# Optimization experiments

Measured on AMD Instinct MI355X. Metric: run time of the kernel, lower is better.

The kernel has to match this reference:

```python
import jax, jax.numpy as jnp
import numpy as np

D_MODEL = 1024
NUM_HEADS = 16
D_K = D_MODEL // NUM_HEADS  # 64
MAX_SEQ_LEN = 2048
THETA = 10000.0
BATCH = 2
SEQ = 2048


def _rope_tables():
    # freqs: [d_k/2], positions: [max_seq_len] -> angles [max_seq_len, d_k/2]
    freqs = THETA ** (-jnp.arange(0, D_K, 2, dtype=jnp.float32) / D_K)
    positions = jnp.arange(MAX_SEQ_LEN, dtype=jnp.float32)[:, None]
    angles = positions * freqs[None, :]
    return jnp.cos(angles), jnp.sin(angles)


def _apply_rope(x, token_positions, cos_cached, sin_cached):
    # x: [..., seq, d_k]; token_positions: [seq]
    cos = cos_cached[token_positions]  # [seq, d_k/2]
    sin = sin_cached[token_positions]
    x_even = x[..., ::2]
    x_odd = x[..., 1::2]
    r_even = x_even * cos - x_odd * sin
    r_odd = x_even * sin + x_odd * cos
    # interleave even/odd back into last dim
    out = jnp.stack([r_even, r_odd], axis=-1)
    return out.reshape(x.shape)


def setup_inputs() -> dict:
    key = jax.random.key(0)
    ks = jax.random.split(key, 5)
    scale = 1.0 / np.sqrt(D_MODEL)
    in_features = jax.random.normal(ks[0], (BATCH, SEQ, D_MODEL), dtype=jnp.float32)
    q_proj = jax.random.normal(ks[1], (D_MODEL, D_MODEL), dtype=jnp.float32) * scale
    k_proj = jax.random.normal(ks[2], (D_MODEL, D_MODEL), dtype=jnp.float32) * scale
    v_proj = jax.random.normal(ks[3], (D_MODEL, D_MODEL), dtype=jnp.float32) * scale
    o_proj = jax.random.normal(ks[4], (D_MODEL, D_MODEL), dtype=jnp.float32) * scale
    mask = jnp.tril(jnp.ones((SEQ, SEQ), dtype=bool))  # causal
    token_positions = jnp.arange(SEQ, dtype=jnp.int32)
    return {
        "in_features": in_features,
        "q_proj": q_proj,
        "k_proj": k_proj,
        "v_proj": v_proj,
        "o_proj": o_proj,
        "mask": mask,
        "token_positions": token_positions,
    }


def reference(in_features, q_proj, k_proj, v_proj, o_proj, mask, token_positions):
    B, S, _ = in_features.shape
    cos_cached, sin_cached = _rope_tables()
    # fused QKV projection (same math as x @ cat(Wq,Wk,Wv).T then chunk)
    q = jnp.einsum("bsd,ed->bse", in_features, q_proj)
    k = jnp.einsum("bsd,ed->bse", in_features, k_proj)
    v = jnp.einsum("bsd,ed->bse", in_features, v_proj)
    # ... seq (h d) -> ... h seq d
    q = q.reshape(B, S, NUM_HEADS, D_K).transpose(0, 2, 1, 3)
    k = k.reshape(B, S, NUM_HEADS, D_K).transpose(0, 2, 1, 3)
    v = v.reshape(B, S, NUM_HEADS, D_K).transpose(0, 2, 1, 3)
    q = _apply_rope(q, token_positions, cos_cached, sin_cached)
    k = _apply_rope(k, token_positions, cos_cached, sin_cached)
    scores = jnp.einsum("bhqd,bhkd->bhqk", q, k) / np.sqrt(D_K)
    scores = jnp.where(mask, scores, -jnp.inf)
    attn = jax.nn.softmax(scores, axis=-1)
    out = jnp.einsum("bhqk,bhkd->bhqd", attn, v)
    # ... h seq d -> ... seq (h d)
    concat = out.transpose(0, 2, 1, 3).reshape(B, S, D_MODEL)
    return jnp.einsum("bsd,ed->bse", concat, o_proj)
```

## Files before the change

### kernel.cpp

```cpp
#include <hip/hip_runtime.h>
#include <cstdint>

#define D_MODEL 1024
#define NHEADS 16
#define DKH 64
#define SEQL 2048
#define NBATCH 2
#define NROWS (NBATCH * SEQL)

typedef __bf16 bf16;
typedef __bf16 bf16x2 __attribute__((ext_vector_type(2)));
typedef __bf16 bf16x4 __attribute__((ext_vector_type(4)));
typedef __bf16 bf16x8 __attribute__((ext_vector_type(8)));
typedef float f32x4 __attribute__((ext_vector_type(4)));
typedef float f32x16 __attribute__((ext_vector_type(16)));
typedef unsigned u32x4 __attribute__((ext_vector_type(4)));

static __device__ __forceinline__ f32x4 mfma16(bf16x8 a, bf16x8 b, f32x4 c) {
  return __builtin_amdgcn_mfma_f32_16x16x32_bf16(a, b, c, 0, 0, 0);
}

static __device__ __forceinline__ f32x16 mfma32(bf16x8 a, bf16x8 b, f32x16 c) {
  return __builtin_amdgcn_mfma_f32_32x32x16_bf16(a, b, c, 0, 0, 0);
}

static __device__ __forceinline__ void gload_lds16(const bf16* g, bf16* l) {
  __builtin_amdgcn_global_load_lds(
      (const __attribute__((address_space(1))) void*)g,
      (__attribute__((address_space(3))) void*)l, 16, 0, 0);
}

static __device__ __forceinline__ float fexp2(float x) {
  return __builtin_amdgcn_exp2f(x);
}

static __device__ __forceinline__ unsigned cvt_pk(float a, float b) {
  unsigned r;
  asm("v_cvt_pk_bf16_f32 %0, %1, %2" : "=v"(r) : "v"(a), "v"(b));
  return r;
}

static __device__ __forceinline__ void plswap(unsigned& a, unsigned& b) {
  asm("v_permlane32_swap_b32 %0, %1" : "+v"(a), "+v"(b));
}

__global__ __launch_bounds__(256) void convert_kernel(
    const float* __restrict__ x, const float* __restrict__ wq,
    const float* __restrict__ wk, const float* __restrict__ wv,
    const float* __restrict__ wo, bf16* __restrict__ xb,
    bf16* __restrict__ wqb, bf16* __restrict__ wkb, bf16* __restrict__ wvb,
    bf16* __restrict__ wob) {
  int i4 = blockIdx.x * 256 + threadIdx.x;
  const float* src;
  bf16* dst;
  int off;
  if (i4 < (NROWS * D_MODEL / 4)) {
    src = x; dst = xb; off = i4;
  } else {
    int j = i4 - NROWS * D_MODEL / 4;
    int sel = j >> 18;
    off = j & ((1 << 18) - 1);
    src = sel == 0 ? wq : sel == 1 ? wk : sel == 2 ? wv : wo;
    dst = sel == 0 ? wqb : sel == 1 ? wkb : sel == 2 ? wvb : wob;
  }
  float4 v = ((const float4*)src)[off];
  bf16x4 o;
  o[0] = (bf16)v.x; o[1] = (bf16)v.y; o[2] = (bf16)v.z; o[3] = (bf16)v.w;
  ((bf16x4*)dst)[off] = o;
}

__global__ __launch_bounds__(256, 3) void qkv_gemm(
    const bf16* __restrict__ A, const bf16* __restrict__ Bq,
    const bf16* __restrict__ Bk, const bf16* __restrict__ Bv,
    const int* __restrict__ tpos, bf16* __restrict__ Qb,
    bf16* __restrict__ Kb, bf16* __restrict__ Vt) {
  __shared__ bf16 As[128 * 64];
  __shared__ bf16 Bs[3][64 * 64];
  const int t = threadIdx.x, wave = t >> 6, lane = t & 63;
  const int quad = lane >> 4, l16 = lane & 15;
  const int bm = blockIdx.x * 128, bn = blockIdx.y * 64;

  f32x4 acc[3][2][4];
  for (int o = 0; o < 3; o++)
    for (int mt = 0; mt < 2; mt++)
      for (int nt = 0; nt < 4; nt++)
        for (int r = 0; r < 4; r++) acc[o][mt][nt][r] = 0.0f;

  for (int k0 = 0; k0 < D_MODEL; k0 += 64) {
    for (int j = 0; j < 4; j++) {
      int s = (wave * 4 + j) * 64 + lane;
      int srow = s >> 3, scol = (s & 7) ^ (srow & 7);
      gload_lds16(&A[(size_t)(bm + srow) * D_MODEL + k0 + scol * 8],
                  &As[(wave * 4 + j) * 512]);
    }
    for (int j = 0; j < 2; j++) {
      int s = (wave * 2 + j) * 64 + lane;
      int srow = s >> 3, scol = (s & 7) ^ (srow & 7);
      size_t goff = (size_t)(bn + srow) * D_MODEL + k0 + scol * 8;
      gload_lds16(&Bq[goff], &Bs[0][(wave * 2 + j) * 512]);
      gload_lds16(&Bk[goff], &Bs[1][(wave * 2 + j) * 512]);
      gload_lds16(&Bv[goff], &Bs[2][(wave * 2 + j) * 512]);
    }
    __syncthreads();
    for (int kh = 0; kh < 2; kh++) {
      const int kc = kh * 4 + quad;
      bf16x8 af[2];
      for (int mt = 0; mt < 2; mt++) {
        int row = wave * 32 + mt * 16 + l16;
        af[mt] = *(bf16x8*)&As[row * 64 + (kc ^ (row & 7)) * 8];
      }
      for (int nt = 0; nt < 4; nt++) {
        int row = nt * 16 + l16;
        int off = row * 64 + (kc ^ (row & 7)) * 8;
        bf16x8 bq = *(bf16x8*)&Bs[0][off];
        bf16x8 bk = *(bf16x8*)&Bs[1][off];
        bf16x8 bv = *(bf16x8*)&Bs[2][off];
        for (int mt = 0; mt < 2; mt++) {
          acc[0][mt][nt] = mfma16(af[mt], bq, acc[0][mt][nt]);
          acc[1][mt][nt] = mfma16(af[mt], bk, acc[1][mt][nt]);
          acc[2][mt][nt] = mfma16(af[mt], bv, acc[2][mt][nt]);
        }
      }
    }
    __syncthreads();
  }

  const float qsc = 0.125f * 1.44269504f;
  float freqv[4], sgn[4];
  for (int nt = 0; nt < 4; nt++) {
    int cp = (bn + nt * 16 + l16) & 63;
    freqv[nt] = fexp2((float)(cp >> 1) * -0.41524101f);
    sgn[nt] = (cp & 1) ? 1.0f : -1.0f;
  }
  for (int mt = 0; mt < 2; mt++) {
    int row0 = bm + wave * 32 + mt * 16 + quad * 4;
    for (int r = 0; r < 4; r++) {
      int row = row0 + r;
      float pos = (float)tpos[row & (SEQL - 1)];
      for (int nt = 0; nt < 4; nt++) {
        int col = bn + nt * 16 + l16;
        float sn, cs;
        __sincosf(pos * freqv[nt], &sn, &cs);
        float vq = acc[0][mt][nt][r];
        float vk = acc[1][mt][nt][r];
        float pq = __shfl_xor(vq, 1);
        float pk = __shfl_xor(vk, 1);
        float rq = vq * cs + sgn[nt] * pq * sn;
        float rk = vk * cs + sgn[nt] * pk * sn;
        Qb[(size_t)row * D_MODEL + col] = (bf16)(rq * qsc);
        Kb[(size_t)row * D_MODEL + col] = (bf16)rk;
      }
    }
    for (int nt = 0; nt < 4; nt++) {
      int col = bn + nt * 16 + l16;
      bf16x4 pv;
      for (int r = 0; r < 4; r++) pv[r] = (bf16)acc[2][mt][nt][r];
      *(bf16x4*)&Vt[(size_t)col * NROWS + row0] = pv;
    }
  }
}

template <int BM, int BN, typename OutT>
__device__ __forceinline__ void gemm_body64(const bf16* __restrict__ A,
                                            const bf16* __restrict__ Bm,
                                            OutT* __restrict__ C, int bm,
                                            int bn, int N, int K) {
  constexpr int MT = BM / 32, NT = BN / 32;
  constexpr int CA = BM / 32, CB = BN / 32;
  __shared__ bf16 As[BM * 64];
  __shared__ bf16 Bs[BN * 64];
  const int t = threadIdx.x;
  const int wave = t >> 6, lane = t & 63;
  const int quad = lane >> 4, l16 = lane & 15;
  const int wm = (wave >> 1) * (MT * 16), wn = (wave & 1) * (NT * 16);

  f32x4 acc[MT][NT];
  for (int i = 0; i < MT; i++)
    for (int j = 0; j < NT; j++)
      for (int r = 0; r < 4; r++) acc[i][j][r] = 0.0f;

  for (int k0 = 0; k0 < K; k0 += 64) {
    for (int j = 0; j < CA; j++) {
      int s = (wave * CA + j) * 64 + lane;
      int srow = s >> 3, scol = (s & 7) ^ (srow & 7);
      gload_lds16(&A[(size_t)(bm + srow) * K + k0 + scol * 8],
                  &As[(wave * CA + j) * 512]);
    }
    for (int j = 0; j < CB; j++) {
      int s = (wave * CB + j) * 64 + lane;
      int srow = s >> 3, scol = (s & 7) ^ (srow & 7);
      gload_lds16(&Bm[(size_t)(bn + srow) * K + k0 + scol * 8],
                  &Bs[(wave * CB + j) * 512]);
    }
    __syncthreads();
    for (int kh = 0; kh < 2; kh++) {
      const int kc = kh * 4 + quad;
      bf16x8 af[MT], bfr[NT];
      for (int mt = 0; mt < MT; mt++) {
        int row = wm + mt * 16 + l16;
        af[mt] = *(bf16x8*)&As[row * 64 + (kc ^ (row & 7)) * 8];
      }
      for (int nt = 0; nt < NT; nt++) {
        int row = wn + nt * 16 + l16;
        bfr[nt] = *(bf16x8*)&Bs[row * 64 + (kc ^ (row & 7)) * 8];
      }
      for (int mt = 0; mt < MT; mt++)
        for (int nt = 0; nt < NT; nt++)
          acc[mt][nt] = mfma16(af[mt], bfr[nt], acc[mt][nt]);
    }
    __syncthreads();
  }
  for (int mt = 0; mt < MT; mt++)
    for (int nt = 0; nt < NT; nt++)
      for (int r = 0; r < 4; r++) {
        int row = bm + wm + mt * 16 + quad * 4 + r;
        int col = bn + wn + nt * 16 + l16;
        C[(size_t)row * N + col] = (OutT)acc[mt][nt][r];
      }
}

__global__ __launch_bounds__(256, 3) void o_gemm(const bf16* __restrict__ A,
                                                 const bf16* __restrict__ Bm,
                                                 float* __restrict__ C) {
  gemm_body64<64, 128, float>(A, Bm, C, blockIdx.x * 64, blockIdx.y * 128,
                              D_MODEL, D_MODEL);
}

__global__ __launch_bounds__(256) void attn_kernel(
    const bf16* __restrict__ Q, const bf16* __restrict__ K,
    const bf16* __restrict__ Vt_g, float* __restrict__ O0,
    float* __restrict__ O1, float* __restrict__ O2, float* __restrict__ O3,
    float* __restrict__ L0, float* __restrict__ L1, float* __restrict__ L2,
    float* __restrict__ L3) {
  const int t = threadIdx.x;
  const int wave = t >> 6, lane = t & 63;
  const int l32 = lane & 31, hi = lane >> 5;

  const int id = blockIdx.x;
  const int bh = id & 31;
  const int c = 39 - (id >> 5);
  int qt, piece, np;
  if (c < 4)       { qt = c;                 piece = 0;            np = 1; }
  else if (c < 12) { int e = c - 4;  qt = 4 + (e >> 1); piece = e & 1; np = 2; }
  else if (c < 24) { int e = c - 12; qt = 8 + e / 3;    piece = e % 3; np = 3; }
  else             { int e = c - 24; qt = 12 + (e >> 2); piece = e & 3; np = 4; }
  const int total = qt + 1, bas = total / np, rem = total % np;
  const int len = bas + (piece < rem ? 1 : 0);
  const int k0 = piece * bas + (piece < rem ? piece : rem);
  const int k1 = k0 + len - 1;

  const int b = bh >> 4, h = bh & 15;
  const int q_base = qt * 128;
  const size_t base = (size_t)b * SEQL * D_MODEL + h * DKH;

  __shared__ bf16 Ks[128 * 64];
  __shared__ bf16 Vts[64 * 128];

  const int r8 = lane >> 3, c8 = lane & 7;
  const int r16 = lane >> 4, c16 = lane & 15;

  for (int i = 0; i < 4; i++) {
    int row = wave * 32 + i * 8 + r8;
    int sc = c8 ^ (row & 7);
    gload_lds16(&Q[base + (size_t)(q_base + row) * D_MODEL + sc * 8],
                &Ks[(wave * 32 + i * 8) * 64]);
  }
  __syncthreads();
  bf16x8 qb[4];
  {
    int row = wave * 32 + l32;
#pragma unroll
    for (int ks = 0; ks < 4; ks++) {
      int ch = (ks * 2 + hi) ^ (row & 7);
      qb[ks] = *(bf16x8*)&Ks[row * 64 + ch * 8];
    }
  }
  __syncthreads();

  f32x16 oaccT[2];
  float lsum = 0.0f;
#pragma unroll
  for (int dt = 0; dt < 2; dt++)
#pragma unroll
    for (int r = 0; r < 16; r++) oaccT[dt][r] = 0.0f;

  const bf16* Vrow0 = &Vt_g[(size_t)(h * 64) * NROWS + b * SEQL];

  for (int kv = k0; kv <= k1; kv++) {
    const int kv_base = kv * 128;
    for (int i = 0; i < 4; i++) {
      int row = wave * 32 + i * 8 + r8;
      int sc = c8 ^ (row & 7);
      gload_lds16(&K[base + (size_t)(kv_base + row) * D_MODEL + sc * 8],
                  &Ks[(wave * 32 + i * 8) * 64]);
    }
    for (int i = 0; i < 4; i++) {
      int d = wave * 16 + i * 4 + r16;
      int sc = c16 ^ (d & 7);
      gload_lds16(&Vrow0[(size_t)d * NROWS + kv_base + sc * 8],
                  &Vts[(wave * 16 + i * 4) * 128]);
    }
    __syncthreads();

    const bool diag = (kv == qt);
#pragma unroll
    for (int cc = 0; cc < 4; cc++) {
      f32x16 sT;
#pragma unroll
      for (int r = 0; r < 16; r++) sT[r] = 0.0f;
      {
        int krow = cc * 32 + l32;
#pragma unroll
        for (int ks = 0; ks < 4; ks++) {
          int ch = (ks * 2 + hi) ^ (krow & 7);
          bf16x8 kf = *(bf16x8*)&Ks[krow * 64 + ch * 8];
          sT = mfma32(kf, qb[ks], sT);
        }
      }
      if (diag) {
        int q_loc = wave * 32 + l32;
#pragma unroll
        for (int r = 0; r < 16; r++) {
          int key = cc * 32 + (r & 3) + 8 * (r >> 2) + 4 * hi;
          if (key > q_loc) sT[r] = -1e30f;
        }
      }
      float p[16];
#pragma unroll
      for (int r = 0; r < 16; r++) p[r] = fexp2(sT[r]);
      lsum += (((p[0] + p[1]) + (p[2] + p[3])) +
               ((p[4] + p[5]) + (p[6] + p[7]))) +
              (((p[8] + p[9]) + (p[10] + p[11])) +
               ((p[12] + p[13]) + (p[14] + p[15])));
      unsigned a0 = cvt_pk(p[0], p[1]),  a1 = cvt_pk(p[2], p[3]);
      unsigned b0 = cvt_pk(p[4], p[5]),  b1 = cvt_pk(p[6], p[7]);
      unsigned c0 = cvt_pk(p[8], p[9]),  c1 = cvt_pk(p[10], p[11]);
      unsigned d0 = cvt_pk(p[12], p[13]), d1 = cvt_pk(p[14], p[15]);
      plswap(a0, b0); plswap(a1, b1); plswap(c0, d0); plswap(c1, d1);
      bf16x8 pf[2];
      {
        u32x4 u = {a0, a1, b0, b1};
        pf[0] = __builtin_bit_cast(bf16x8, u);
      }
      {
        u32x4 u = {c0, c1, d0, d1};
        pf[1] = __builtin_bit_cast(bf16x8, u);
      }
#pragma unroll
      for (int dt = 0; dt < 2; dt++) {
        int d = dt * 32 + l32;
#pragma unroll
        for (int ks = 0; ks < 2; ks++) {
          int ch = (cc * 4 + ks * 2 + hi) ^ (d & 7);
          bf16x8 vf = *(bf16x8*)&Vts[d * 128 + ch * 8];
          oaccT[dt] = mfma32(vf, pf[ks], oaccT[dt]);
        }
      }
    }
    __syncthreads();
  }

  lsum += __shfl_xor(lsum, 32);
  float* Ob;
  float* Lb;
  int rbase, roff;
  if (piece == 0)      { Ob = O0; Lb = L0; rbase = SEQL;        roff = 0; }
  else if (piece == 1) { Ob = O1; Lb = L1; rbase = SEQL - 512;  roff = 512; }
  else if (piece == 2) { Ob = O2; Lb = L2; rbase = SEQL - 1024; roff = 1024; }
  else                 { Ob = O3; Lb = L3; rbase = SEQL - 1536; roff = 1536; }
  {
    int qrow = q_base + wave * 32 + l32;
    size_t orow = (size_t)b * rbase + (qrow - roff);
    if (hi == 0) Lb[orow * NHEADS + h] = lsum;
#pragma unroll
    for (int dt = 0; dt < 2; dt++)
#pragma unroll
      for (int rq = 0; rq < 4; rq++) {
        f32x4 vv = {oaccT[dt][rq * 4 + 0], oaccT[dt][rq * 4 + 1],
                    oaccT[dt][rq * 4 + 2], oaccT[dt][rq * 4 + 3]};
        *(f32x4*)&Ob[orow * D_MODEL + h * DKH + dt * 32 + rq * 8 + hi * 4] =
            vv;
      }
  }
}

__global__ __launch_bounds__(256) void normalize_kernel(
    const float* __restrict__ O0, const float* __restrict__ O1,
    const float* __restrict__ O2, const float* __restrict__ O3,
    const float* __restrict__ L0, const float* __restrict__ L1,
    const float* __restrict__ L2, const float* __restrict__ L3,
    bf16* __restrict__ Cc) {
  int i4 = blockIdx.x * 256 + threadIdx.x;
  int row = i4 >> 8;
  int c0 = (i4 & 255) * 4;
  int s = row & (SEQL - 1);
  int b = row >> 11;
  int h = c0 >> 6;
  float l = L0[(size_t)row * NHEADS + h];
  f32x4 v = *(const f32x4*)&O0[(size_t)row * D_MODEL + c0];
  if (s >= 512) {
    size_t r1 = (size_t)b * (SEQL - 512) + (s - 512);
    l += L1[r1 * NHEADS + h];
    f32x4 u = *(const f32x4*)&O1[r1 * D_MODEL + c0];
    for (int r = 0; r < 4; r++) v[r] += u[r];
  }
  if (s >= 1024) {
    size_t r2 = (size_t)b * (SEQL - 1024) + (s - 1024);
    l += L2[r2 * NHEADS + h];
    f32x4 u = *(const f32x4*)&O2[r2 * D_MODEL + c0];
    for (int r = 0; r < 4; r++) v[r] += u[r];
  }
  if (s >= 1536) {
    size_t r3 = (size_t)b * (SEQL - 1536) + (s - 1536);
    l += L3[r3 * NHEADS + h];
    f32x4 u = *(const f32x4*)&O3[r3 * D_MODEL + c0];
    for (int r = 0; r < 4; r++) v[r] += u[r];
  }
  float inv = 1.0f / l;
  bf16x4 o;
  o[0] = (bf16)(v[0] * inv);
  o[1] = (bf16)(v[1] * inv);
  o[2] = (bf16)(v[2] * inv);
  o[3] = (bf16)(v[3] * inv);
  *(bf16x4*)&Cc[(size_t)row * D_MODEL + c0] = o;
}

extern "C" void kernel_launch(void* const* d_in, const int* in_sizes, int n_in,
                              void* d_out, int out_size, void* d_ws,
                              size_t ws_size, hipStream_t stream) {
  const float* x = (const float*)d_in[0];
  const float* wq = (const float*)d_in[1];
  const float* wk = (const float*)d_in[2];
  const float* wv = (const float*)d_in[3];
  const float* wo = (const float*)d_in[4];
  const int* tpos = (const int*)d_in[6];
  float* out = (float*)d_out;

  char* p = (char*)d_ws;
  bf16* xb  = (bf16*)p; p += (size_t)NROWS * D_MODEL * 2;
  bf16* wqb = (bf16*)p; p += (size_t)D_MODEL * D_MODEL * 2;
  bf16* wkb = (bf16*)p; p += (size_t)D_MODEL * D_MODEL * 2;
  bf16* wvb = (bf16*)p; p += (size_t)D_MODEL * D_MODEL * 2;
  bf16* wob = (bf16*)p; p += (size_t)D_MODEL * D_MODEL * 2;
  bf16* Qb  = (bf16*)p; p += (size_t)NROWS * D_MODEL * 2;
  bf16* Kb  = (bf16*)p; p += (size_t)NROWS * D_MODEL * 2;
  bf16* Vt  = (bf16*)p; p += (size_t)NROWS * D_MODEL * 2;
  bf16* Cc  = (bf16*)p; p += (size_t)NROWS * D_MODEL * 2;
  float* O0 = (float*)p; p += (size_t)NROWS * D_MODEL * 4;
  float* L0 = (float*)p; p += (size_t)NROWS * NHEADS * 4;
  float* O1 = (float*)p; p += (size_t)NBATCH * (SEQL - 512) * D_MODEL * 4;
  float* L1 = (float*)p; p += (size_t)NBATCH * (SEQL - 512) * NHEADS * 4;
  float* O2 = (float*)xb;
  float* O3 = (float*)wqb;
  float* L2 = (float*)wvb;
  float* L3 = (float*)wvb + (size_t)NBATCH * (SEQL - 1024) * NHEADS;

  convert_kernel<<<8192, 256, 0, stream>>>(x, wq, wk, wv, wo, xb, wqb, wkb,
                                           wvb, wob);
  qkv_gemm<<<dim3(NROWS / 128, D_MODEL / 64), 256, 0, stream>>>(
      xb, wqb, wkb, wvb, tpos, Qb, Kb, Vt);
  attn_kernel<<<1280, 256, 0, stream>>>(Qb, Kb, Vt, O0, O1, O2, O3, L0, L1,
                                        L2, L3);
  normalize_kernel<<<NROWS * D_MODEL / 1024, 256, 0, stream>>>(
      O0, O1, O2, O3, L0, L1, L2, L3, Cc);
  o_gemm<<<dim3(NROWS / 64, D_MODEL / 128), 256, 0, stream>>>(Cc, wob, out);
}
```

Baseline: 183.9 us.

## Double-buffer K/V in LDS with 64-key chunks to overlap loads and MFMA

The attention inner loop now processes 64-key half tiles instead of 128-key tiles. It keeps two LDS buffers for K and V and issues the next chunk's global-to-LDS loads before computing on the current one. Explicit vmcnt waits and raw s_barrier replace the per-iteration __syncthreads pair. The aim is to hide global load latency behind the QK and PV MFMAs. In exchange there are twice as many barriers per key tile, and the hand-set vmcnt counts must stay in step with the load count per stage.

```diff
diff --git a/kernel.cpp b/kernel.cpp
--- a/kernel.cpp
+++ b/kernel.cpp
@@ -247,23 +247,20 @@
   const int total = qt + 1, bas = total / np, rem = total % np;
   const int len = bas + (piece < rem ? 1 : 0);
   const int k0 = piece * bas + (piece < rem ? piece : rem);
-  const int k1 = k0 + len - 1;
 
   const int b = bh >> 4, h = bh & 15;
   const int q_base = qt * 128;
   const size_t base = (size_t)b * SEQL * D_MODEL + h * DKH;
 
-  __shared__ bf16 Ks[128 * 64];
-  __shared__ bf16 Vts[64 * 128];
+  __shared__ bf16 lds[16384];
 
   const int r8 = lane >> 3, c8 = lane & 7;
-  const int r16 = lane >> 4, c16 = lane & 15;
 
   for (int i = 0; i < 4; i++) {
     int row = wave * 32 + i * 8 + r8;
     int sc = c8 ^ (row & 7);
     gload_lds16(&Q[base + (size_t)(q_base + row) * D_MODEL + sc * 8],
-                &Ks[(wave * 32 + i * 8) * 64]);
+                &lds[(wave * 32 + i * 8) * 64]);
   }
   __syncthreads();
   bf16x8 qb[4];
@@ -272,7 +269,7 @@
 #pragma unroll
     for (int ks = 0; ks < 4; ks++) {
       int ch = (ks * 2 + hi) ^ (row & 7);
-      qb[ks] = *(bf16x8*)&Ks[row * 64 + ch * 8];
+      qb[ks] = *(bf16x8*)&lds[row * 64 + ch * 8];
     }
   }
   __syncthreads();
@@ -285,26 +282,43 @@
     for (int r = 0; r < 16; r++) oaccT[dt][r] = 0.0f;
 
   const bf16* Vrow0 = &Vt_g[(size_t)(h * 64) * NROWS + b * SEQL];
-
-  for (int kv = k0; kv <= k1; kv++) {
-    const int kv_base = kv * 128;
-    for (int i = 0; i < 4; i++) {
-      int row = wave * 32 + i * 8 + r8;
+  const int q_glob = q_base + wave * 32 + l32;
+
+  auto stage = [&](int hc) {
+    int buf = hc & 1;
+    int kb = k0 * 128 + hc * 64;
+#pragma unroll
+    for (int i = 0; i < 2; i++) {
+      int seg = wave * 2 + i;
+      int row = seg * 8 + r8;
       int sc = c8 ^ (row & 7);
-      gload_lds16(&K[base + (size_t)(kv_base + row) * D_MODEL + sc * 8],
-                  &Ks[(wave * 32 + i * 8) * 64]);
-    }
-    for (int i = 0; i < 4; i++) {
-      int d = wave * 16 + i * 4 + r16;
-      int sc = c16 ^ (d & 7);
-      gload_lds16(&Vrow0[(size_t)d * NROWS + kv_base + sc * 8],
-                  &Vts[(wave * 16 + i * 4) * 128]);
-    }
-    __syncthreads();
-
-    const bool diag = (kv == qt);
-#pragma unroll
-    for (int cc = 0; cc < 4; cc++) {
+      gload_lds16(&K[base + (size_t)(kb + row) * D_MODEL + sc * 8],
+                  &lds[buf * 4096 + seg * 512]);
+      gload_lds16(&Vrow0[(size_t)row * NROWS + kb + sc * 8],
+                  &lds[8192 + buf * 4096 + seg * 512]);
+    }
+  };
+
+  const int nch = 2 * len;
+  stage(0);
+  for (int hc = 0; hc < nch; hc++) {
+    if (hc + 1 < nch) {
+      stage(hc + 1);
+      asm volatile("s_waitcnt vmcnt(4)" ::: "memory");
+    } else {
+      asm volatile("s_waitcnt vmcnt(0)" ::: "memory");
+    }
+    __builtin_amdgcn_sched_barrier(0);
+    __builtin_amdgcn_s_barrier();
+
+    const int buf = hc & 1;
+    const bf16* Kb_ = &lds[buf * 4096];
+    const bf16* Vb_ = &lds[8192 + buf * 4096];
+    const int kb = k0 * 128 + hc * 64;
+    const bool diag = ((kb >> 7) == qt);
+
+#pragma unroll
+    for (int cc = 0; cc < 2; cc++) {
       f32x16 sT;
 #pragma unroll
       for (int r = 0; r < 16; r++) sT[r] = 0.0f;
@@ -313,16 +327,15 @@
 #pragma unroll
         for (int ks = 0; ks < 4; ks++) {
           int ch = (ks * 2 + hi) ^ (krow & 7);
-          bf16x8 kf = *(bf16x8*)&Ks[krow * 64 + ch * 8];
+          bf16x8 kf = *(bf16x8*)&Kb_[krow * 64 + ch * 8];
           sT = mfma32(kf, qb[ks], sT);
         }
       }
       if (diag) {
-        int q_loc = wave * 32 + l32;
 #pragma unroll
         for (int r = 0; r < 16; r++) {
-          int key = cc * 32 + (r & 3) + 8 * (r >> 2) + 4 * hi;
-          if (key > q_loc) sT[r] = -1e30f;
+          int key = kb + cc * 32 + (r & 3) + 8 * (r >> 2) + 4 * hi;
+          if (key > q_glob) sT[r] = -1e30f;
         }
       }
       float p[16];
@@ -352,12 +365,14 @@
 #pragma unroll
         for (int ks = 0; ks < 2; ks++) {
           int ch = (cc * 4 + ks * 2 + hi) ^ (d & 7);
-          bf16x8 vf = *(bf16x8*)&Vts[d * 128 + ch * 8];
+          bf16x8 vf = *(bf16x8*)&Vb_[d * 64 + ch * 8];
           oaccT[dt] = mfma32(vf, pf[ks], oaccT[dt]);
         }
       }
     }
-    __syncthreads();
+    asm volatile("" ::: "memory");
+    __builtin_amdgcn_sched_barrier(0);
+    __builtin_amdgcn_s_barrier();
   }
 
   lsum += __shfl_xor(lsum, 32);
```

After: 184.2 us. Within noise of the previous version (+0.1%).

## Read K and V fragments directly from global memory instead of LDS staging

Applied to the files above, without the earlier changes.

The attention kernel stops staging K and V tiles into shared memory and removes the per-tile barriers. Each wave now loads its MFMA operands straight from global memory (through the caches), and s_setprio is raised around the MFMA sections. This avoids the LDS round trip and the block-wide synchronisation. The cost is redundant global/L2 traffic, since all four waves read the same K/V tiles, plus load latency exposed directly to the MFMAs without explicit prefetch.

```diff
diff --git a/kernel.cpp b/kernel.cpp
--- a/kernel.cpp
+++ b/kernel.cpp
@@ -253,17 +253,15 @@
   const int q_base = qt * 128;
   const size_t base = (size_t)b * SEQL * D_MODEL + h * DKH;
 
-  __shared__ bf16 Ks[128 * 64];
-  __shared__ bf16 Vts[64 * 128];
+  __shared__ bf16 Qs[128 * 64];
 
   const int r8 = lane >> 3, c8 = lane & 7;
-  const int r16 = lane >> 4, c16 = lane & 15;
 
   for (int i = 0; i < 4; i++) {
     int row = wave * 32 + i * 8 + r8;
     int sc = c8 ^ (row & 7);
     gload_lds16(&Q[base + (size_t)(q_base + row) * D_MODEL + sc * 8],
-                &Ks[(wave * 32 + i * 8) * 64]);
+                &Qs[(wave * 32 + i * 8) * 64]);
   }
   __syncthreads();
   bf16x8 qb[4];
@@ -272,10 +270,9 @@
 #pragma unroll
     for (int ks = 0; ks < 4; ks++) {
       int ch = (ks * 2 + hi) ^ (row & 7);
-      qb[ks] = *(bf16x8*)&Ks[row * 64 + ch * 8];
-    }
-  }
-  __syncthreads();
+      qb[ks] = *(bf16x8*)&Qs[row * 64 + ch * 8];
+    }
+  }
 
   f32x16 oaccT[2];
   float lsum = 0.0f;
@@ -284,45 +281,34 @@
 #pragma unroll
     for (int r = 0; r < 16; r++) oaccT[dt][r] = 0.0f;
 
-  const bf16* Vrow0 = &Vt_g[(size_t)(h * 64) * NROWS + b * SEQL];
+  const bf16* Kp = &K[base];
+  const bf16* Vp = &Vt_g[(size_t)(h * 64) * NROWS + b * SEQL];
+  const int q_glob = q_base + wave * 32 + l32;
 
   for (int kv = k0; kv <= k1; kv++) {
     const int kv_base = kv * 128;
-    for (int i = 0; i < 4; i++) {
-      int row = wave * 32 + i * 8 + r8;
-      int sc = c8 ^ (row & 7);
-      gload_lds16(&K[base + (size_t)(kv_base + row) * D_MODEL + sc * 8],
-                  &Ks[(wave * 32 + i * 8) * 64]);
-    }
-    for (int i = 0; i < 4; i++) {
-      int d = wave * 16 + i * 4 + r16;
-      int sc = c16 ^ (d & 7);
-      gload_lds16(&Vrow0[(size_t)d * NROWS + kv_base + sc * 8],
-                  &Vts[(wave * 16 + i * 4) * 128]);
-    }
-    __syncthreads();
-
     const bool diag = (kv == qt);
 #pragma unroll
     for (int cc = 0; cc < 4; cc++) {
+      const int key0 = kv_base + cc * 32;
       f32x16 sT;
 #pragma unroll
       for (int r = 0; r < 16; r++) sT[r] = 0.0f;
       {
-        int krow = cc * 32 + l32;
+        const bf16* krowp = &Kp[(size_t)(key0 + l32) * D_MODEL + hi * 8];
+        __builtin_amdgcn_s_setprio(1);
 #pragma unroll
         for (int ks = 0; ks < 4; ks++) {
-          int ch = (ks * 2 + hi) ^ (krow & 7);
-          bf16x8 kf = *(bf16x8*)&Ks[krow * 64 + ch * 8];
+          bf16x8 kf = *(const bf16x8*)&krowp[ks * 16];
           sT = mfma32(kf, qb[ks], sT);
         }
+        __builtin_amdgcn_s_setprio(0);
       }
       if (diag) {
-        int q_loc = wave * 32 + l32;
 #pragma unroll
         for (int r = 0; r < 16; r++) {
-          int key = cc * 32 + (r & 3) + 8 * (r >> 2) + 4 * hi;
-          if (key > q_loc) sT[r] = -1e30f;
+          int key = key0 + (r & 3) + 8 * (r >> 2) + 4 * hi;
+          if (key > q_glob) sT[r] = -1e30f;
         }
       }
       float p[16];
@@ -346,18 +332,18 @@
         u32x4 u = {c0, c1, d0, d1};
         pf[1] = __builtin_bit_cast(bf16x8, u);
       }
+      __builtin_amdgcn_s_setprio(1);
 #pragma unroll
       for (int dt = 0; dt < 2; dt++) {
-        int d = dt * 32 + l32;
+        const bf16* vrowp = &Vp[(size_t)(dt * 32 + l32) * NROWS + key0 + hi * 8];
 #pragma unroll
         for (int ks = 0; ks < 2; ks++) {
-          int ch = (cc * 4 + ks * 2 + hi) ^ (d & 7);
-          bf16x8 vf = *(bf16x8*)&Vts[d * 128 + ch * 8];
+          bf16x8 vf = *(const bf16x8*)&vrowp[ks * 16];
           oaccT[dt] = mfma32(vf, pf[ks], oaccT[dt]);
         }
       }
-    }
-    __syncthreads();
+      __builtin_amdgcn_s_setprio(0);
+    }
   }
 
   lsum += __shfl_xor(lsum, 32);
```

Result: slower. 234.0 us (+27.2%).
